# Kernel optimization log

Measured on AMD Instinct MI355X. Metric: run time of the kernel, lower is better.

Reference implementation:

```python
import jax, jax.numpy as jnp
import numpy as np

N = 200_000        # primal nodes (mesh faces)
E = 600_000        # directed primal edges (= dual nodes)
F = 128            # feature dim
NUM_KEEP = 300_000 # num_primal_edges_to_keep
ITERS = 40         # label-propagation iterations (>= ~2*log2(N), safely converged)


def setup_inputs() -> dict:
    key = jax.random.key(0)
    k1, k2, k3, k4 = jax.random.split(key, 4)
    primal_x = jax.random.normal(k1, (N, F), dtype=jnp.float32)
    dual_x = jax.random.normal(k2, (E, F), dtype=jnp.float32)
    att = jax.random.uniform(k3, (E,), dtype=jnp.float32)  # attention coeffs in (0,1)
    primal_edge_index = jax.random.randint(k4, (2, E), 0, N, dtype=jnp.int32)
    return {"primal_x": primal_x, "dual_x": dual_x, "att": att,
            "primal_edge_index": primal_edge_index}


def _pool(primal_x, dual_x, att, primal_edge_index):
    src, dst = primal_edge_index[0], primal_edge_index[1]
    num_pool = E - NUM_KEEP

    # --- Top-K edge selection by decreasing attention coefficient ---
    order = jnp.argsort(-att)
    pool_mask = jnp.zeros((E,), jnp.bool_).at[order[:num_pool]].set(True)

    # --- Union-find / connected components of pooled edges via
    #     min-label propagation with pointer jumping (vectorized union-find) ---
    u = src
    v = jnp.where(pool_mask, dst, src)  # masked edges become self-edges (no-ops)

    def body(_, l):
        l = l.at[u].min(l[v]).at[v].min(l[u])  # edge relaxations (scatter-min)
        l = l[l]                                # pointer jumping
        l = l[l]
        return l

    labels = jax.lax.fori_loop(0, ITERS, body, jnp.arange(N, dtype=jnp.int32))

    # --- Compact component labels into contiguous new-primal-node ids ---
    _, cluster = jnp.unique(labels, size=N, fill_value=N, return_inverse=True)
    cluster = cluster.astype(jnp.int32)

    # --- Aggregate primal node features per cluster ('mean') ---
    counts = jax.ops.segment_sum(jnp.ones((N,), primal_x.dtype), cluster,
                                 num_segments=N)
    new_primal_x = jax.ops.segment_sum(primal_x, cluster, num_segments=N)
    new_primal_x = new_primal_x / jnp.maximum(counts, 1.0)[:, None]

    # --- Rebuild primal edges; edges internal to a cluster are pooled away ---
    cu, cv = cluster[src], cluster[dst]
    valid = cu != cv
    new_primal_edge_index = jnp.stack([jnp.where(valid, cu, -1),
                                       jnp.where(valid, cv, -1)])

    # --- Dual nodes: one per (unordered) surviving new primal edge
    #     ('single' dual nodes); merge & mean-aggregate dual features of old
    #     dual nodes mapping to the same new dual node ---
    a = jnp.minimum(cu, cv)
    b = jnp.maximum(cu, cv)
    pairs = jnp.stack([jnp.where(valid, a, N), jnp.where(valid, b, N)], axis=1)
    _, dual_cluster = jnp.unique(pairs, axis=0, size=E, fill_value=N,
                                 return_inverse=True)
    dual_cluster = dual_cluster.reshape(E).astype(jnp.int32)
    vm = valid.astype(dual_x.dtype)
    dcounts = jax.ops.segment_sum(vm, dual_cluster, num_segments=E)
    new_dual_x = jax.ops.segment_sum(dual_x * vm[:, None], dual_cluster,
                                     num_segments=E)
    new_dual_x = new_dual_x / jnp.maximum(dcounts, 1.0)[:, None]

    return new_primal_x, new_dual_x, new_primal_edge_index, cluster


def reference(primal_x, dual_x, att, primal_edge_index):
    return _pool(primal_x, dual_x, att, primal_edge_index)
```

## Files before the change

kernel.cpp:

```cpp
#include <hip/hip_runtime.h>
#include <stdint.h>


#define N_NODES 200000
#define N_EDGES 600000
#define FDIM 128
#define NUM_POOL 300000u

#define SC_NEEDEQ 3
#define SC_TIECNT 4
#define SC_C 5
#define SC_W 6
#define SC_U 7
#define SC_VCNT 8
#define SC_WL0 16
#define TIECAP 4096
#define WLCAP 300800
#define HB 256
#define NSB 98
#define NSHAD 8
#define NSHAD2 16
#define CMAX 16384
#define SROWS 128
#define SGB 391
#define CS2B 128

__device__ __forceinline__ uint32_t f2ou(float f){
  uint32_t b = __float_as_uint(f);
  return (b & 0x80000000u) ? ~b : (b | 0x80000000u);
}

static __device__ __forceinline__ void sel_level(const uint32_t* hist, uint32_t& target,
                                                 uint32_t& pfx, uint32_t* sm, uint32_t* res){
  int t = threadIdx.x;
  uint32_t cnt = hist[t];
  sm[t] = cnt; __syncthreads();
  for(int off = 1; off < 256; off <<= 1){
    uint32_t y = (t + off < 256) ? sm[t + off] : 0u;
    __syncthreads(); sm[t] += y; __syncthreads();
  }
  uint32_t suffix = sm[t];
  uint32_t above  = suffix - cnt;
  if(above < target && target <= suffix){ res[0] = (uint32_t)t; res[1] = target - above; }
  __syncthreads();
  pfx = (pfx << 8) | res[0];
  target = res[1];
  __syncthreads();
}

static __device__ __forceinline__ uint32_t blk_excl(uint32_t v, uint32_t* sm, uint32_t& total){
  int t = threadIdx.x;
  sm[t] = v; __syncthreads();
  for(int off = 1; off < 256; off <<= 1){
    uint32_t y = (t >= off) ? sm[t - off] : 0u;
    __syncthreads(); sm[t] += y; __syncthreads();
  }
  total = sm[255];
  uint32_t incl = sm[t];
  __syncthreads();
  return incl - v;
}

__global__ __launch_bounds__(256) void k_zero(uint4* w4, uint32_t n4){
  uint32_t gid = blockIdx.x*256 + threadIdx.x;
  uint4 z = make_uint4(0u,0u,0u,0u);
  for(uint32_t j = gid; j < n4; j += gridDim.x*256) w4[j] = z;
}

template<int LEVEL>
__global__ __launch_bounds__(256) void k_hist8(const float* att, uint32_t* hists, int* L){
  __shared__ uint32_t h[256];
  __shared__ uint32_t sm[256];
  __shared__ uint32_t res[2];
  h[threadIdx.x] = 0;
  if(LEVEL == 1){
    for(int i = blockIdx.x*256 + threadIdx.x; i < N_NODES; i += HB*256) L[i] = i;
  }
  __syncthreads();
  uint32_t pfx = 0, target = NUM_POOL;
  #pragma unroll
  for(int l = 0; l < LEVEL-1; ++l) sel_level(hists + 256*l, target, pfx, sm, res);
  constexpr int SH1 = (LEVEL > 1) ? 8*(5-LEVEL) : 0;
  constexpr int SH2 = 8*(4-LEVEL);
  for(int e = blockIdx.x*256 + threadIdx.x; e < N_EDGES; e += HB*256){
    uint32_t u = f2ou(att[e]);
    bool ok = (LEVEL == 1) || ((u >> SH1) == pfx);
    if(ok) atomicAdd(&h[(u >> SH2) & 0xFFu], 1u);
  }
  __syncthreads();
  uint32_t c = h[threadIdx.x];
  if(c) atomicAdd(&hists[256*(LEVEL-1) + threadIdx.x], c);
}

__global__ __launch_bounds__(256) void k_seed(const float* att, const int* src, const int* dst,
                       const uint32_t* hists, uint32_t* sc, uint32_t* tieIdx, int* L, uint2* wl){
  __shared__ uint32_t sm[256];
  __shared__ uint32_t res[2];
  __shared__ uint32_t basesh;
  uint32_t pfx = 0, target = NUM_POOL;
  #pragma unroll
  for(int l = 0; l < 4; ++l) sel_level(hists + 256*l, target, pfx, sm, res);
  if(blockIdx.x == 0 && threadIdx.x == 0) sc[SC_NEEDEQ] = target;
  uint32_t T = pfx;
  int e = blockIdx.x*256 + threadIdx.x;
  bool app = false; int u = 0, v = 0;
  if(e < N_EDGES){
    uint32_t ub = f2ou(att[e]);
    if(ub > T){
      u = src[e]; v = dst[e];
      if(u != v){
        int m = u < v ? u : v, hi = u ^ v ^ m;
        atomicMin(&L[hi], m);
        app = true;
      }
    } else if(ub == T){
      uint32_t p = atomicAdd(&sc[SC_TIECNT], 1u);
      if(p < TIECAP) tieIdx[p] = (uint32_t)e;
    }
  }
  uint32_t tot;
  uint32_t off = blk_excl(app ? 1u : 0u, sm, tot);
  if(threadIdx.x == 0 && tot) basesh = atomicAdd(&sc[SC_WL0], tot);
  __syncthreads();
  if(app) wl[basesh + off] = make_uint2((uint32_t)(u < v ? u : v), (uint32_t)(u > v ? u : v));
}
__global__ __launch_bounds__(1024) void k_tiesel(uint32_t* sc, const uint32_t* tieIdx,
                        const int* src, const int* dst, int* L, uint2* wl){
  uint32_t m = sc[SC_TIECNT]; if(m > TIECAP) m = TIECAP;
  uint32_t need = sc[SC_NEEDEQ];
  int lane = threadIdx.x & 63;
  for(uint32_t i0 = 0; i0 < m; i0 += 1024){
    uint32_t i = i0 + threadIdx.x;
    bool app = false; int u = 0, v = 0;
    if(i < m){
      uint32_t mine = tieIdx[i];
      uint32_t r = 0;
      for(uint32_t j = 0; j < m; j++) r += (tieIdx[j] < mine) ? 1u : 0u;
      if(r < need){
        u = src[mine]; v = dst[mine];
        if(u != v){ int mm = u < v ? u : v, hi = u ^ v ^ mm; atomicMin(&L[hi], mm); app = true; }
      }
    }
    unsigned long long grp = __ballot(app);
    if(grp){
      int leader = __ffsll(grp) - 1;
      uint32_t base = 0;
      if(lane == leader) base = atomicAdd(&sc[SC_WL0], (uint32_t)__popcll(grp));
      base = (uint32_t)__shfl((int)base, leader);
      if(app){
        uint32_t off = (uint32_t)__popcll(grp & ((1ull << lane) - 1ull));
        wl[base + off] = make_uint2((uint32_t)(u < v ? u : v), (uint32_t)(u > v ? u : v));
      }
    }
  }
}
__global__ __launch_bounds__(256) void k_relax(const uint2* wl_in, uint2* wl_out, int* L,
                       uint32_t* sc, int inSlot, int outSlot){
  __shared__ uint32_t sm[256];
  __shared__ uint32_t basesh;
  uint32_t n = sc[inSlot];
  for(uint32_t base = blockIdx.x*256u; base < n; base += gridDim.x*256u){
    uint32_t idx = base + threadIdx.x;
    bool active = idx < n;
    int lu = 0, lv = 0;
    if(active){
      uint2 ed = wl_in[idx];
      lu = L[ed.x]; lu = L[lu]; lu = L[lu]; lu = L[lu];
      lv = L[ed.y]; lv = L[lv]; lv = L[lv]; lv = L[lv];
      active = (lu != lv);
      if(active){
        int m = lu < lv ? lu : lv, hi = lu ^ lv ^ m;
        atomicMin(&L[hi], m);
      }
    }
    uint32_t tot;
    uint32_t off = blk_excl(active ? 1u : 0u, sm, tot);
    if(threadIdx.x == 0 && tot) basesh = atomicAdd(&sc[outSlot], tot);
    __syncthreads();
    if(active) wl_out[basesh + off] = make_uint2((uint32_t)(lu < lv ? lu : lv),
                                                 (uint32_t)(lu > lv ? lu : lv));
  }
  if(n != 0){
    int i = blockIdx.x*256 + threadIdx.x;
    if(i < N_NODES){
      int v = L[i]; v = L[v]; v = L[v]; v = L[v];
      if(v < i) atomicMin(&L[i], v);
    }
  }
}
__global__ __launch_bounds__(256) void k_flatten_reduce(int* L, uint32_t* bsums){
  uint32_t base = blockIdx.x*2048u + threadIdx.x*8u;
  uint32_t s = 0;
  #pragma unroll
  for(int k = 0; k < 8; k++){
    uint32_t i = base + k;
    if(i < N_NODES){
      int p = L[i]; int q = L[p];
      while(q != p){ p = q; q = L[p]; }
      L[i] = p;
      s += (p == (int)i) ? 1u : 0u;
    }
  }
  __shared__ uint32_t sm[256];
  sm[threadIdx.x] = s; __syncthreads();
  for(int off = 128; off > 0; off >>= 1){
    if((int)threadIdx.x < off) sm[threadIdx.x] += sm[threadIdx.x + off];
    __syncthreads();
  }
  if(threadIdx.x == 0) bsums[blockIdx.x] = sm[0];
}

template<int MODE>
__device__ __forceinline__ uint32_t scan_n(const uint32_t* sc){
  if(MODE == 1) return sc[SC_W];
  if(MODE == 3) return sc[SC_C]*NSHAD2;
  return N_NODES;
}
template<int MODE>
__global__ __launch_bounds__(256) void k_scan_reduce(const uint32_t* in, uint32_t* bsums,
                       const uint32_t* sc, float* dsum, uint32_t* dcnt){
  uint32_t n = scan_n<MODE>(sc);
  if(MODE == 1){
    uint32_t vc = sc[SC_VCNT];
    size_t gid = (size_t)blockIdx.x*256 + threadIdx.x, gs = (size_t)gridDim.x*256;
    float4* d4 = (float4*)dsum;
    float4 z = make_float4(0.f,0.f,0.f,0.f);
    for(size_t j = gid; j < (size_t)vc*(FDIM/4); j += gs) d4[j] = z;
    for(size_t j = gid; j < vc; j += gs) dcnt[j] = 0u;
  }
  uint32_t base = blockIdx.x*2048u + threadIdx.x*8u;
  uint32_t s = 0;
  #pragma unroll
  for(int k = 0; k < 8; k++){
    uint32_t idx = base + k;
    if(idx < n){ uint32_t v = in[idx]; if(MODE == 1) v = __popc(v); s += v; }
  }
  __shared__ uint32_t sm[256];
  sm[threadIdx.x] = s; __syncthreads();
  for(int off = 128; off > 0; off >>= 1){
    if((int)threadIdx.x < off) sm[threadIdx.x] += sm[threadIdx.x + off];
    __syncthreads();
  }
  if(threadIdx.x == 0) bsums[blockIdx.x] = sm[0];
}
template<int MODE>
__global__ __launch_bounds__(256) void k_scan_apply(const uint32_t* in, const int* L,
                       const uint32_t* bsums, int nb, uint32_t* out, uint32_t* sc){
  __shared__ uint32_t bs[4096];
  __shared__ uint32_t sm[256];
  int t = threadIdx.x;
  uint32_t n = scan_n<MODE>(sc);
  uint32_t loc[16]; uint32_t ls = 0;
  #pragma unroll
  for(int k = 0; k < 16; k++){ int idx = t*16 + k; uint32_t v = (idx < nb) ? bsums[idx] : 0u; loc[k] = v; ls += v; }
  sm[t] = ls; __syncthreads();
  for(int off = 1; off < 256; off <<= 1){
    uint32_t y = (t >= off) ? sm[t - off] : 0u;
    __syncthreads(); sm[t] += y; __syncthreads();
  }
  uint32_t total = sm[255];
  uint32_t run = sm[t] - ls;
  #pragma unroll
  for(int k = 0; k < 16; k++){ bs[t*16 + k] = run; run += loc[k]; }
  __syncthreads();
  uint32_t blockbase = bs[blockIdx.x];
  __syncthreads();
  uint32_t base = blockIdx.x*2048u + t*8u;
  uint32_t xs[8]; uint32_t ts2 = 0;
  #pragma unroll
  for(int k = 0; k < 8; k++){
    uint32_t idx = base + k; uint32_t v = 0;
    if(idx < n){
      if(MODE == 2) v = (L[idx] == (int)idx) ? 1u : 0u;
      else { v = in[idx]; if(MODE == 1) v = __popc(v); }
    }
    xs[k] = v; ts2 += v;
  }
  sm[t] = ts2; __syncthreads();
  for(int off = 1; off < 256; off <<= 1){
    uint32_t y = (t >= off) ? sm[t - off] : 0u;
    __syncthreads(); sm[t] += y; __syncthreads();
  }
  uint32_t run2 = blockbase + sm[t] - ts2;
  #pragma unroll
  for(int k = 0; k < 8; k++){ uint32_t idx = base + k; if(idx < n) out[idx] = run2; run2 += xs[k]; }
  if(blockIdx.x == 0 && t == 0){
    if(MODE == 2){ sc[SC_C] = total; uint64_t cc = (uint64_t)total*(uint64_t)total; sc[SC_W] = (uint32_t)((cc + 31ull) >> 5); }
    if(MODE == 1){ sc[SC_U] = total; }
  }
}

__global__ __launch_bounds__(256) void k_cluster_counts(const int* L, const uint32_t* rank_,
                       int* cluster_i, float* outC, uint32_t* counts, uint32_t* counts2,
                       float* psumS, uint32_t* bitmap, const uint32_t* sc){
  uint32_t C = sc[SC_C], W = sc[SC_W];
  uint32_t gid = blockIdx.x*256 + threadIdx.x, gs = gridDim.x*256;
  float4* p4 = (float4*)psumS;
  float4 z = make_float4(0.f,0.f,0.f,0.f);
  for(size_t j = gid; j < (size_t)NSHAD*C*(FDIM/4); j += gs) p4[j] = z;
  for(uint32_t j = gid; j < W; j += gs) bitmap[j] = 0u;
  int i = (int)gid;
  int lane = threadIdx.x & 63;
  int sh = (int)((gid >> 6) & (NSHAD2-1));
  int c = -1;
  if(i < N_NODES){
    c = (int)rank_[L[i]];
    cluster_i[i] = c;
    outC[i] = (float)c;
  }
  unsigned long long remaining = __ballot(i < N_NODES);
  while(remaining){
    int leader = __ffsll(remaining) - 1;
    int lc = __shfl(c, leader);
    unsigned long long grp = __ballot(c == lc) & remaining;
    if(lane == leader){
      uint32_t cnt = (uint32_t)__popcll(grp);
      atomicAdd(&counts[lc], cnt);
      atomicAdd(&counts2[lc*NSHAD2 + sh], cnt);
    }
    remaining &= ~grp;
  }
}
__global__ void k_scatter(const int* cluster_i, uint32_t* cursor2, uint32_t* order){
  uint32_t gid = blockIdx.x*256 + threadIdx.x;
  int i = (int)gid;
  int lane = threadIdx.x & 63;
  int sh = (int)((gid >> 6) & (NSHAD2-1));
  int c = (i < N_NODES) ? cluster_i[i] : -1;
  unsigned long long remaining = __ballot(i < N_NODES);
  while(remaining){
    int leader = __ffsll(remaining) - 1;
    int lc = __shfl(c, leader);
    unsigned long long grp = __ballot(c == lc) & remaining;
    int b = 0;
    if(lane == leader) b = (int)atomicAdd(&cursor2[lc*NSHAD2 + sh], (uint32_t)__popcll(grp));
    b = __shfl(b, leader);
    if((grp >> lane) & 1ull){
      uint32_t sub = (uint32_t)__popcll(grp & ((1ull << lane) - 1ull));
      order[(uint32_t)b + sub] = (uint32_t)i;
    }
    remaining &= ~grp;
  }
}

__global__ __launch_bounds__(256) void k_seg_edges(const float* px, const uint32_t* order,
        const int* cluster_i, float* psumS, const int* src, const int* dst, uint32_t* sc,
        float* outE, uint32_t* kc, uint32_t* bitmap){
  if(blockIdx.x < SGB){
    int wave = (int)((blockIdx.x*256u + threadIdx.x) >> 6);
    int lane = threadIdx.x & 63;
    int start = wave * SROWS;
    if(start >= N_NODES) return;
    int cnt = N_NODES - start; if(cnt > SROWS) cnt = SROWS;
    size_t shadBase = (size_t)(wave & (NSHAD-1)) * (size_t)sc[SC_C] * FDIM;
    uint32_t ord0 = 0, ord1 = 0; int c0 = -1, c1 = -1;
    if(lane < cnt){ ord0 = order[start + lane]; c0 = cluster_i[ord0]; }
    if(64 + lane < cnt){ ord1 = order[start + 64 + lane]; c1 = cluster_i[ord1]; }
    float ax = 0.f, ay = 0.f; int cur = -1;
    for(int r = 0; r < cnt; r++){
      uint32_t i; int c;
      if(r < 64){ i = (uint32_t)__shfl((int)ord0, r); c = __shfl(c0, r); }
      else      { i = (uint32_t)__shfl((int)ord1, r - 64); c = __shfl(c1, r - 64); }
      if(c != cur){
        if(cur >= 0){
          atomicAdd(&psumS[shadBase + (size_t)cur*FDIM + 2*lane], ax);
          atomicAdd(&psumS[shadBase + (size_t)cur*FDIM + 2*lane + 1], ay);
        }
        cur = c; ax = 0.f; ay = 0.f;
      }
      float2 v = ((const float2*)(px + (size_t)i*FDIM))[lane];
      ax += v.x; ay += v.y;
    }
    if(cur >= 0){
      atomicAdd(&psumS[shadBase + (size_t)cur*FDIM + 2*lane], ax);
      atomicAdd(&psumS[shadBase + (size_t)cur*FDIM + 2*lane + 1], ay);
    }
  } else {
    __shared__ uint32_t wsum[4];
    int e = (blockIdx.x - SGB)*256 + threadIdx.x;
    int lane = threadIdx.x & 63;
    int wv = threadIdx.x >> 6;
    bool val = false;
    if(e < N_EDGES){
      int cu = cluster_i[src[e]];
      int cv = cluster_i[dst[e]];
      val = (cu != cv);
      outE[e] = val ? (float)cu : -1.0f;
      outE[N_EDGES + e] = val ? (float)cv : -1.0f;
      if(val){
        int a = cu < cv ? cu : cv, b = cu < cv ? cv : cu;
        uint32_t C = sc[SC_C];
        uint32_t key = (uint32_t)a * C + (uint32_t)b;
        kc[e] = key;
        atomicOr(&bitmap[key >> 5], 1u << (key & 31u));
      } else {
        kc[e] = 0xFFFFFFFFu;
      }
    }
    unsigned long long grp = __ballot(val);
    if(lane == 0) wsum[wv] = (uint32_t)__popcll(grp);
    __syncthreads();
    if(threadIdx.x == 0){
      uint32_t s = wsum[0] + wsum[1] + wsum[2] + wsum[3];
      if(s) atomicAdd(&sc[SC_VCNT], s);
    }
  }
}

__global__ __launch_bounds__(256) void k_dualacc(const float* dx, const uint32_t* kc,
                          const uint32_t* bitmap, const uint32_t* wpref,
                          float* dsum, uint32_t* dcnt){
  int wave = (int)((blockIdx.x*256u + threadIdx.x) >> 6);
  int lane = threadIdx.x & 63;
  int base = wave * 64;
  if(base >= N_EDGES) return;
  int e = base + lane;
  uint32_t key = (e < N_EDGES) ? kc[e] : 0xFFFFFFFFu;
  bool val = (key != 0xFFFFFFFFu);
  uint32_t r = 0;
  if(val){
    uint32_t wi = key >> 5, bi = key & 31u;
    r = wpref[wi] + __popc(bitmap[wi] & ((1u << bi) - 1u));
  }
  unsigned long long m = __ballot(val);
  while(m){
    int b = __ffsll(m) - 1;
    m &= m - 1;
    uint32_t ee = (uint32_t)(base + b);
    uint32_t rr = (uint32_t)__shfl((int)r, b);
    float2 v = ((const float2*)(dx + (size_t)ee*FDIM))[lane];
    atomicAdd(&dsum[(size_t)rr*FDIM + 2*lane], v.x);
    atomicAdd(&dsum[(size_t)rr*FDIM + 2*lane + 1], v.y);
    if(lane == 0) atomicAdd(&dcnt[rr], 1u);
  }
}
__global__ __launch_bounds__(256) void k_finalize(const float4* psumS, const uint32_t* counts,
        const float4* dsum, const uint32_t* dcnt, const uint32_t* sc, float4* out4){
  uint32_t C = sc[SC_C], U = sc[SC_U];
  size_t cs = (size_t)C * (FDIM/4);
  size_t gid = (size_t)blockIdx.x*256 + threadIdx.x;
  size_t gs = (size_t)gridDim.x*256;
  const size_t NP4 = (size_t)N_NODES*(FDIM/4);
  const size_t TOT4 = (size_t)(N_NODES + N_EDGES)*(FDIM/4);
  for(size_t j = gid; j < TOT4; j += gs){
    float4 v = make_float4(0.f,0.f,0.f,0.f);
    if(j < NP4){
      uint32_t r = (uint32_t)(j >> 5);
      if(r < C){
        v = psumS[j];
        #pragma unroll
        for(int s = 1; s < NSHAD; s++){
          float4 t = psumS[(size_t)s*cs + j];
          v.x += t.x; v.y += t.y; v.z += t.z; v.w += t.w;
        }
        float fc = (float)counts[r];
        v.x /= fc; v.y /= fc; v.z /= fc; v.w /= fc;
      }
    } else {
      size_t dj = j - NP4;
      uint32_t r = (uint32_t)(dj >> 5);
      if(r < U){
        v = dsum[dj];
        float fc = (float)dcnt[r];
        v.x /= fc; v.y /= fc; v.z /= fc; v.w /= fc;
      }
    }
    out4[j] = v;
  }
}

extern "C" void kernel_launch(void* const* d_in, const int* in_sizes, int n_in,
                              void* d_out, int out_size, void* d_ws, size_t ws_size,
                              hipStream_t stream){
  (void)in_sizes; (void)n_in; (void)out_size;
  const float* primal_x = (const float*)d_in[0];
  const float* dual_x   = (const float*)d_in[1];
  const float* att      = (const float*)d_in[2];
  const int*   pei      = (const int*)d_in[3];
  const int* src = pei;
  const int* dst = pei + N_EDGES;

  float* out  = (float*)d_out;
  float* outE = out + (size_t)(N_NODES + N_EDGES)*FDIM;
  float* outC = outE + (size_t)2*N_EDGES;

  uint32_t* w = (uint32_t*)d_ws;
  size_t words_avail = ws_size / 4;
  const size_t PSUMW = (size_t)NSHAD*CMAX*FDIM;
  const size_t CNT2W = (size_t)CMAX*NSHAD2;
  const size_t FIXED = 64 + 1024 + (size_t)N_NODES + CNT2W
                     + TIECAP + 4*(size_t)N_NODES + CNT2W + 4*(size_t)WLCAP
                     + (size_t)N_EDGES + (size_t)N_EDGES
                     + 4096
                     + PSUMW + (size_t)N_EDGES*FDIM;
  size_t wcap = (words_avail > FIXED) ? (words_avail - FIXED)/2 : 4;
  if(wcap > 8388608) wcap = 8388608;
  wcap &= ~(size_t)3;

  size_t o = 0;
  uint32_t* sc      = w;               o += 64;
  uint32_t* hists   = w + o;           o += 1024;
  uint32_t* counts  = w + o;           o += N_NODES;
  uint32_t* counts2 = w + o;           o += CNT2W;
  size_t zero_words = o;
  uint32_t* tieIdx  = w + o;           o += TIECAP;
  int* labels       = (int*)(w + o);   o += N_NODES;
  uint32_t* rank_   = w + o;           o += N_NODES;
  int* cluster_i    = (int*)(w + o);   o += N_NODES;
  uint32_t* order   = w + o;           o += N_NODES;
  uint32_t* cursor2 = w + o;           o += CNT2W;
  uint2* wl0        = (uint2*)(w + o); o += 2*(size_t)WLCAP;
  uint2* wl1        = (uint2*)(w + o); o += 2*(size_t)WLCAP;
  uint32_t* kc      = w + o;           o += N_EDGES;
  uint32_t* dcnt    = w + o;           o += N_EDGES;
  uint32_t* bsums   = w + o;           o += 4096;
  float* psumS      = (float*)(w + o); o += PSUMW;
  float* dsum       = (float*)(w + o); o += (size_t)N_EDGES*FDIM;
  uint32_t* bitmap  = w + o;           o += wcap;
  uint32_t* wpref   = w + o;           o += wcap;

  const int EB  = (N_EDGES + 255)/256;
  const int NB  = (N_NODES + 255)/256;
  const int WSB = (int)((wcap + 2047)/2048);

  k_zero<<<128,256,0,stream>>>((uint4*)w, (uint32_t)(zero_words/4));
  k_hist8<1><<<HB,256,0,stream>>>(att, hists, labels);
  k_hist8<2><<<HB,256,0,stream>>>(att, hists, labels);
  k_hist8<3><<<HB,256,0,stream>>>(att, hists, labels);
  k_hist8<4><<<HB,256,0,stream>>>(att, hists, labels);
  k_seed<<<EB,256,0,stream>>>(att, src, dst, hists, sc, tieIdx, labels, wl0);
  k_tiesel<<<1,1024,0,stream>>>(sc, tieIdx, src, dst, labels, wl0);
  for(int r = 1; r <= 8; ++r){
    uint2* win  = (r & 1) ? wl0 : wl1;
    uint2* wout = (r & 1) ? wl1 : wl0;
    k_relax<<<1024,256,0,stream>>>(win, wout, labels, sc, SC_WL0 + r - 1, SC_WL0 + r);
  }
  k_flatten_reduce<<<NSB,256,0,stream>>>(labels, bsums);
  k_scan_apply<2><<<NSB,256,0,stream>>>(counts, labels, bsums, NSB, rank_, sc);
  k_cluster_counts<<<NB,256,0,stream>>>(labels, rank_, cluster_i, outC, counts, counts2,
                                        psumS, bitmap, sc);
  k_scan_reduce<3><<<CS2B,256,0,stream>>>(counts2, bsums, sc, dsum, dcnt);
  k_scan_apply<3><<<CS2B,256,0,stream>>>(counts2, labels, bsums, CS2B, cursor2, sc);
  k_scatter<<<NB,256,0,stream>>>(cluster_i, cursor2, order);
  k_seg_edges<<<SGB + EB,256,0,stream>>>(primal_x, order, cluster_i, psumS,
                                         src, dst, sc, outE, kc, bitmap);
  k_scan_reduce<1><<<WSB,256,0,stream>>>(bitmap, bsums, sc, dsum, dcnt);
  k_scan_apply<1><<<WSB,256,0,stream>>>(bitmap, labels, bsums, WSB, wpref, sc);
  k_dualacc<<<EB,256,0,stream>>>(dual_x, kc, bitmap, wpref, dsum, dcnt);
  k_finalize<<<2048,256,0,stream>>>((const float4*)psumS, counts, (const float4*)dsum,
                                    dcnt, sc, (float4*)out);
}
```

Measured before the change: 626.6 us.

## Fuse seed, union-find relaxation, labeling and scatter into one cooperative kernel

Replaces the chain of small kernels (seed, tie selection, eight relax rounds, flatten, rank scan, cluster counts, count scan, scatter) with a single cooperative persistent kernel of 1024 blocks that uses grid-wide syncs between phases. The aim is to remove roughly fifteen kernel launches and their inter-kernel gaps, and to exit the relax loop early once the worklist is empty. In exchange it adds grid.sync barriers, serial single-block phases for tie selection and the small scans, and it depends on all 1024 blocks being co-resident for the cooperative launch.

```diff
diff --git a/kernel.cpp b/kernel.cpp
--- a/kernel.cpp
+++ b/kernel.cpp
@@ -1,5 +1,8 @@
 #include <hip/hip_runtime.h>
+#include <hip/hip_cooperative_groups.h>
 #include <stdint.h>
+
+namespace cg = cooperative_groups;
 
 
 #define N_NODES 200000
@@ -23,11 +26,14 @@
 #define CMAX 16384
 #define SROWS 128
 #define SGB 391
-#define CS2B 128
+#define CGB 1024
 
 __device__ __forceinline__ uint32_t f2ou(float f){
   uint32_t b = __float_as_uint(f);
   return (b & 0x80000000u) ? ~b : (b | 0x80000000u);
+}
+__device__ __forceinline__ uint32_t ld_ag(const uint32_t* p){
+  return __hip_atomic_load(p, __ATOMIC_RELAXED, __HIP_MEMORY_SCOPE_AGENT);
 }
 
 static __device__ __forceinline__ void sel_level(const uint32_t* hist, uint32_t& target,
@@ -92,135 +98,244 @@
   if(c) atomicAdd(&hists[256*(LEVEL-1) + threadIdx.x], c);
 }
 
-__global__ __launch_bounds__(256) void k_seed(const float* att, const int* src, const int* dst,
-                       const uint32_t* hists, uint32_t* sc, uint32_t* tieIdx, int* L, uint2* wl){
+__global__ __launch_bounds__(256) void k_mega(const float* att, const int* src, const int* dst,
+      const uint32_t* hists, uint32_t* sc, uint32_t* tieIdx, int* L,
+      uint2* wl0, uint2* wl1, uint32_t* bsums, uint32_t* rank_, int* cluster_i,
+      float* outC, uint32_t* counts, uint32_t* counts2, float* psumS,
+      uint32_t* bitmap, uint32_t* cursor2, uint32_t* order){
+  cg::grid_group grid = cg::this_grid();
   __shared__ uint32_t sm[256];
   __shared__ uint32_t res[2];
   __shared__ uint32_t basesh;
+  const uint32_t tid = threadIdx.x;
+  const uint32_t gid = blockIdx.x*256u + tid;
+  const uint32_t GS  = CGB*256u;
+  const int lane = (int)(tid & 63);
+
   uint32_t pfx = 0, target = NUM_POOL;
   #pragma unroll
   for(int l = 0; l < 4; ++l) sel_level(hists + 256*l, target, pfx, sm, res);
-  if(blockIdx.x == 0 && threadIdx.x == 0) sc[SC_NEEDEQ] = target;
-  uint32_t T = pfx;
-  int e = blockIdx.x*256 + threadIdx.x;
-  bool app = false; int u = 0, v = 0;
-  if(e < N_EDGES){
-    uint32_t ub = f2ou(att[e]);
-    if(ub > T){
-      u = src[e]; v = dst[e];
-      if(u != v){
-        int m = u < v ? u : v, hi = u ^ v ^ m;
-        atomicMin(&L[hi], m);
-        app = true;
-      }
-    } else if(ub == T){
-      uint32_t p = atomicAdd(&sc[SC_TIECNT], 1u);
-      if(p < TIECAP) tieIdx[p] = (uint32_t)e;
-    }
-  }
-  uint32_t tot;
-  uint32_t off = blk_excl(app ? 1u : 0u, sm, tot);
-  if(threadIdx.x == 0 && tot) basesh = atomicAdd(&sc[SC_WL0], tot);
-  __syncthreads();
-  if(app) wl[basesh + off] = make_uint2((uint32_t)(u < v ? u : v), (uint32_t)(u > v ? u : v));
-}
-__global__ __launch_bounds__(1024) void k_tiesel(uint32_t* sc, const uint32_t* tieIdx,
-                        const int* src, const int* dst, int* L, uint2* wl){
-  uint32_t m = sc[SC_TIECNT]; if(m > TIECAP) m = TIECAP;
-  uint32_t need = sc[SC_NEEDEQ];
-  int lane = threadIdx.x & 63;
-  for(uint32_t i0 = 0; i0 < m; i0 += 1024){
-    uint32_t i = i0 + threadIdx.x;
+  if(gid == 0) sc[SC_NEEDEQ] = target;
+  const uint32_t T = pfx;
+
+  for(uint32_t e0 = blockIdx.x*256u; e0 < N_EDGES; e0 += GS){
+    uint32_t e = e0 + tid;
     bool app = false; int u = 0, v = 0;
-    if(i < m){
-      uint32_t mine = tieIdx[i];
-      uint32_t r = 0;
-      for(uint32_t j = 0; j < m; j++) r += (tieIdx[j] < mine) ? 1u : 0u;
-      if(r < need){
-        u = src[mine]; v = dst[mine];
-        if(u != v){ int mm = u < v ? u : v, hi = u ^ v ^ mm; atomicMin(&L[hi], mm); app = true; }
-      }
-    }
-    unsigned long long grp = __ballot(app);
-    if(grp){
-      int leader = __ffsll(grp) - 1;
-      uint32_t base = 0;
-      if(lane == leader) base = atomicAdd(&sc[SC_WL0], (uint32_t)__popcll(grp));
-      base = (uint32_t)__shfl((int)base, leader);
-      if(app){
-        uint32_t off = (uint32_t)__popcll(grp & ((1ull << lane) - 1ull));
-        wl[base + off] = make_uint2((uint32_t)(u < v ? u : v), (uint32_t)(u > v ? u : v));
-      }
-    }
-  }
-}
-__global__ __launch_bounds__(256) void k_relax(const uint2* wl_in, uint2* wl_out, int* L,
-                       uint32_t* sc, int inSlot, int outSlot){
-  __shared__ uint32_t sm[256];
-  __shared__ uint32_t basesh;
-  uint32_t n = sc[inSlot];
-  for(uint32_t base = blockIdx.x*256u; base < n; base += gridDim.x*256u){
-    uint32_t idx = base + threadIdx.x;
-    bool active = idx < n;
-    int lu = 0, lv = 0;
-    if(active){
-      uint2 ed = wl_in[idx];
-      lu = L[ed.x]; lu = L[lu]; lu = L[lu]; lu = L[lu];
-      lv = L[ed.y]; lv = L[lv]; lv = L[lv]; lv = L[lv];
-      active = (lu != lv);
+    if(e < N_EDGES){
+      uint32_t ub = f2ou(att[e]);
+      if(ub > T){
+        u = src[e]; v = dst[e];
+        if(u != v){ int m = u < v ? u : v, hi = u ^ v ^ m; atomicMin(&L[hi], m); app = true; }
+      } else if(ub == T){
+        uint32_t p = atomicAdd(&sc[SC_TIECNT], 1u);
+        if(p < TIECAP) tieIdx[p] = e;
+      }
+    }
+    uint32_t tot, off = blk_excl(app ? 1u : 0u, sm, tot);
+    if(tid == 0 && tot) basesh = atomicAdd(&sc[SC_WL0], tot);
+    __syncthreads();
+    if(app) wl0[basesh + off] = make_uint2((uint32_t)(u < v ? u : v), (uint32_t)(u > v ? u : v));
+    __syncthreads();
+  }
+  grid.sync();
+
+  if(blockIdx.x == 0){
+    uint32_t m = sc[SC_TIECNT]; if(m > TIECAP) m = TIECAP;
+    uint32_t need = sc[SC_NEEDEQ];
+    for(uint32_t i0 = 0; i0 < m; i0 += 256){
+      uint32_t i = i0 + tid;
+      bool app = false; int u = 0, v = 0;
+      if(i < m){
+        uint32_t mine = tieIdx[i];
+        uint32_t rr = 0;
+        for(uint32_t j = 0; j < m; j++) rr += (tieIdx[j] < mine) ? 1u : 0u;
+        if(rr < need){
+          u = src[mine]; v = dst[mine];
+          if(u != v){ int mm = u < v ? u : v, hi = u ^ v ^ mm; atomicMin(&L[hi], mm); app = true; }
+        }
+      }
+      uint32_t tot, off = blk_excl(app ? 1u : 0u, sm, tot);
+      if(tid == 0 && tot) basesh = atomicAdd(&sc[SC_WL0], tot);
+      __syncthreads();
+      if(app) wl0[basesh + off] = make_uint2((uint32_t)(u < v ? u : v), (uint32_t)(u > v ? u : v));
+      __syncthreads();
+    }
+  }
+  grid.sync();
+
+  for(int r = 1; r <= 8; ++r){
+    uint32_t n = ld_ag(&sc[SC_WL0 + r - 1]);
+    if(n == 0) break;
+    const uint2* win = (r & 1) ? wl0 : wl1;
+    uint2* wout      = (r & 1) ? wl1 : wl0;
+    for(uint32_t base = blockIdx.x*256u; base < n; base += GS){
+      uint32_t idx = base + tid;
+      bool active = idx < n;
+      int lu = 0, lv = 0;
       if(active){
-        int m = lu < lv ? lu : lv, hi = lu ^ lv ^ m;
-        atomicMin(&L[hi], m);
-      }
-    }
-    uint32_t tot;
-    uint32_t off = blk_excl(active ? 1u : 0u, sm, tot);
-    if(threadIdx.x == 0 && tot) basesh = atomicAdd(&sc[outSlot], tot);
-    __syncthreads();
-    if(active) wl_out[basesh + off] = make_uint2((uint32_t)(lu < lv ? lu : lv),
+        uint2 ed = win[idx];
+        lu = L[ed.x]; lu = L[lu]; lu = L[lu]; lu = L[lu];
+        lv = L[ed.y]; lv = L[lv]; lv = L[lv]; lv = L[lv];
+        active = (lu != lv);
+        if(active){ int m = lu < lv ? lu : lv, hi = lu ^ lv ^ m; atomicMin(&L[hi], m); }
+      }
+      uint32_t tot, off = blk_excl(active ? 1u : 0u, sm, tot);
+      if(tid == 0 && tot) basesh = atomicAdd(&sc[SC_WL0 + r], tot);
+      __syncthreads();
+      if(active) wout[basesh + off] = make_uint2((uint32_t)(lu < lv ? lu : lv),
                                                  (uint32_t)(lu > lv ? lu : lv));
-  }
-  if(n != 0){
-    int i = blockIdx.x*256 + threadIdx.x;
-    if(i < N_NODES){
+      __syncthreads();
+    }
+    for(uint32_t i = gid; i < N_NODES; i += GS){
       int v = L[i]; v = L[v]; v = L[v]; v = L[v];
-      if(v < i) atomicMin(&L[i], v);
-    }
-  }
-}
-__global__ __launch_bounds__(256) void k_flatten_reduce(int* L, uint32_t* bsums){
-  uint32_t base = blockIdx.x*2048u + threadIdx.x*8u;
-  uint32_t s = 0;
-  #pragma unroll
-  for(int k = 0; k < 8; k++){
-    uint32_t i = base + k;
-    if(i < N_NODES){
-      int p = L[i]; int q = L[p];
-      while(q != p){ p = q; q = L[p]; }
-      L[i] = p;
-      s += (p == (int)i) ? 1u : 0u;
-    }
-  }
-  __shared__ uint32_t sm[256];
-  sm[threadIdx.x] = s; __syncthreads();
-  for(int off = 128; off > 0; off >>= 1){
-    if((int)threadIdx.x < off) sm[threadIdx.x] += sm[threadIdx.x + off];
-    __syncthreads();
-  }
-  if(threadIdx.x == 0) bsums[blockIdx.x] = sm[0];
-}
-
-template<int MODE>
-__device__ __forceinline__ uint32_t scan_n(const uint32_t* sc){
-  if(MODE == 1) return sc[SC_W];
-  if(MODE == 3) return sc[SC_C]*NSHAD2;
-  return N_NODES;
-}
-template<int MODE>
-__global__ __launch_bounds__(256) void k_scan_reduce(const uint32_t* in, uint32_t* bsums,
+      if(v < (int)i) atomicMin(&L[i], v);
+    }
+    grid.sync();
+  }
+
+  for(uint32_t chunk = blockIdx.x; chunk < NSB; chunk += CGB){
+    uint32_t base = chunk*2048u + tid*8u;
+    uint32_t s = 0;
+    #pragma unroll
+    for(int k = 0; k < 8; k++){
+      uint32_t i = base + k;
+      if(i < N_NODES){
+        int p = L[i]; int q = L[p];
+        while(q != p){ p = q; q = L[p]; }
+        L[i] = p;
+        s += (p == (int)i) ? 1u : 0u;
+      }
+    }
+    sm[tid] = s; __syncthreads();
+    for(int off = 128; off > 0; off >>= 1){
+      if((int)tid < off) sm[tid] += sm[tid + off];
+      __syncthreads();
+    }
+    if(tid == 0) bsums[chunk] = sm[0];
+    __syncthreads();
+  }
+  grid.sync();
+
+  if(blockIdx.x == 0){
+    uint32_t v = (tid < NSB) ? bsums[tid] : 0u;
+    uint32_t tot, excl = blk_excl(v, sm, tot);
+    if(tid < NSB) bsums[tid] = excl;
+    if(tid == 0){ sc[SC_C] = tot; uint64_t cc = (uint64_t)tot*tot; sc[SC_W] = (uint32_t)((cc + 31ull) >> 5); }
+  }
+  grid.sync();
+
+  for(uint32_t chunk = blockIdx.x; chunk < NSB; chunk += CGB){
+    uint32_t base = chunk*2048u + tid*8u;
+    uint32_t xs[8]; uint32_t ts = 0;
+    #pragma unroll
+    for(int k = 0; k < 8; k++){
+      uint32_t idx = base + k;
+      uint32_t v = (idx < N_NODES && L[idx] == (int)idx) ? 1u : 0u;
+      xs[k] = v; ts += v;
+    }
+    uint32_t tot, excl = blk_excl(ts, sm, tot);
+    uint32_t run = bsums[chunk] + excl;
+    #pragma unroll
+    for(int k = 0; k < 8; k++){ uint32_t idx = base + k; if(idx < N_NODES) rank_[idx] = run; run += xs[k]; }
+    __syncthreads();
+  }
+  grid.sync();
+
+  {
+    uint32_t C = ld_ag(&sc[SC_C]);
+    uint32_t W = ld_ag(&sc[SC_W]);
+    float4* p4 = (float4*)psumS;
+    float4 z = make_float4(0.f,0.f,0.f,0.f);
+    for(size_t j = gid; j < (size_t)NSHAD*C*(FDIM/4); j += GS) p4[j] = z;
+    for(uint32_t j = gid; j < W; j += GS) bitmap[j] = 0u;
+  }
+  for(uint32_t base = blockIdx.x*256u; base < N_NODES; base += GS){
+    uint32_t i0 = base + tid;
+    bool act = i0 < N_NODES;
+    int c = -1;
+    if(act){
+      c = (int)rank_[L[i0]];
+      cluster_i[i0] = c;
+      outC[i0] = (float)c;
+    }
+    int sh = (int)((i0 >> 6) & (NSHAD2-1));
+    unsigned long long remaining = __ballot(act);
+    while(remaining){
+      int leader = __ffsll(remaining) - 1;
+      int lc = __shfl(c, leader);
+      unsigned long long grp = __ballot(c == lc) & remaining;
+      if(lane == leader){
+        uint32_t cnt = (uint32_t)__popcll(grp);
+        atomicAdd(&counts[lc], cnt);
+        atomicAdd(&counts2[lc*NSHAD2 + sh], cnt);
+      }
+      remaining &= ~grp;
+    }
+  }
+  grid.sync();
+
+  uint32_t C = ld_ag(&sc[SC_C]);
+  uint32_t n2 = C*NSHAD2;
+  uint32_t nch = (n2 + 2047u) >> 11;
+  for(uint32_t chunk = blockIdx.x; chunk < nch; chunk += CGB){
+    uint32_t base = chunk*2048u + tid*8u;
+    uint32_t s = 0;
+    #pragma unroll
+    for(int k = 0; k < 8; k++){ uint32_t idx = base + k; if(idx < n2) s += counts2[idx]; }
+    sm[tid] = s; __syncthreads();
+    for(int off = 128; off > 0; off >>= 1){
+      if((int)tid < off) sm[tid] += sm[tid + off];
+      __syncthreads();
+    }
+    if(tid == 0) bsums[chunk] = sm[0];
+    __syncthreads();
+  }
+  grid.sync();
+  if(blockIdx.x == 0){
+    uint32_t v = (tid < nch) ? bsums[tid] : 0u;
+    uint32_t tot, excl = blk_excl(v, sm, tot);
+    if(tid < nch) bsums[tid] = excl;
+  }
+  grid.sync();
+  for(uint32_t chunk = blockIdx.x; chunk < nch; chunk += CGB){
+    uint32_t base = chunk*2048u + tid*8u;
+    uint32_t xs[8]; uint32_t ts = 0;
+    #pragma unroll
+    for(int k = 0; k < 8; k++){ uint32_t idx = base + k; uint32_t v = (idx < n2) ? counts2[idx] : 0u; xs[k] = v; ts += v; }
+    uint32_t tot, excl = blk_excl(ts, sm, tot);
+    uint32_t run = bsums[chunk] + excl;
+    #pragma unroll
+    for(int k = 0; k < 8; k++){ uint32_t idx = base + k; if(idx < n2) cursor2[idx] = run; run += xs[k]; }
+    __syncthreads();
+  }
+  grid.sync();
+
+  for(uint32_t base = blockIdx.x*256u; base < N_NODES; base += GS){
+    uint32_t i0 = base + tid;
+    bool act = i0 < N_NODES;
+    int c = act ? cluster_i[i0] : -1;
+    int sh = (int)((i0 >> 6) & (NSHAD2-1));
+    unsigned long long remaining = __ballot(act);
+    while(remaining){
+      int leader = __ffsll(remaining) - 1;
+      int lc = __shfl(c, leader);
+      unsigned long long grp = __ballot(c == lc) & remaining;
+      int b = 0;
+      if(lane == leader) b = (int)atomicAdd(&cursor2[lc*NSHAD2 + sh], (uint32_t)__popcll(grp));
+      b = __shfl(b, leader);
+      if((grp >> lane) & 1ull){
+        uint32_t sub = (uint32_t)__popcll(grp & ((1ull << lane) - 1ull));
+        order[(uint32_t)b + sub] = i0;
+      }
+      remaining &= ~grp;
+    }
+  }
+}
+
+__global__ __launch_bounds__(256) void k_scan_reduce1(const uint32_t* in, uint32_t* bsums,
                        const uint32_t* sc, float* dsum, uint32_t* dcnt){
-  uint32_t n = scan_n<MODE>(sc);
-  if(MODE == 1){
+  uint32_t n = sc[SC_W];
+  {
     uint32_t vc = sc[SC_VCNT];
     size_t gid = (size_t)blockIdx.x*256 + threadIdx.x, gs = (size_t)gridDim.x*256;
     float4* d4 = (float4*)dsum;
@@ -233,7 +348,7 @@
   #pragma unroll
   for(int k = 0; k < 8; k++){
     uint32_t idx = base + k;
-    if(idx < n){ uint32_t v = in[idx]; if(MODE == 1) v = __popc(v); s += v; }
+    if(idx < n) s += __popc(in[idx]);
   }
   __shared__ uint32_t sm[256];
   sm[threadIdx.x] = s; __syncthreads();
@@ -243,13 +358,12 @@
   }
   if(threadIdx.x == 0) bsums[blockIdx.x] = sm[0];
 }
-template<int MODE>
-__global__ __launch_bounds__(256) void k_scan_apply(const uint32_t* in, const int* L,
-                       const uint32_t* bsums, int nb, uint32_t* out, uint32_t* sc){
+__global__ __launch_bounds__(256) void k_scan_apply1(const uint32_t* in, const uint32_t* bsums,
+                       int nb, uint32_t* out, uint32_t* sc){
   __shared__ uint32_t bs[4096];
   __shared__ uint32_t sm[256];
   int t = threadIdx.x;
-  uint32_t n = scan_n<MODE>(sc);
+  uint32_t n = sc[SC_W];
   uint32_t loc[16]; uint32_t ls = 0;
   #pragma unroll
   for(int k = 0; k < 16; k++){ int idx = t*16 + k; uint32_t v = (idx < nb) ? bsums[idx] : 0u; loc[k] = v; ls += v; }
@@ -269,11 +383,8 @@
   uint32_t xs[8]; uint32_t ts2 = 0;
   #pragma unroll
   for(int k = 0; k < 8; k++){
-    uint32_t idx = base + k; uint32_t v = 0;
-    if(idx < n){
-      if(MODE == 2) v = (L[idx] == (int)idx) ? 1u : 0u;
-      else { v = in[idx]; if(MODE == 1) v = __popc(v); }
-    }
+    uint32_t idx = base + k;
+    uint32_t v = (idx < n) ? __popc(in[idx]) : 0u;
     xs[k] = v; ts2 += v;
   }
   sm[t] = ts2; __syncthreads();
@@ -284,63 +395,7 @@
   uint32_t run2 = blockbase + sm[t] - ts2;
   #pragma unroll
   for(int k = 0; k < 8; k++){ uint32_t idx = base + k; if(idx < n) out[idx] = run2; run2 += xs[k]; }
-  if(blockIdx.x == 0 && t == 0){
-    if(MODE == 2){ sc[SC_C] = total; uint64_t cc = (uint64_t)total*(uint64_t)total; sc[SC_W] = (uint32_t)((cc + 31ull) >> 5); }
-    if(MODE == 1){ sc[SC_U] = total; }
-  }
-}
-
-__global__ __launch_bounds__(256) void k_cluster_counts(const int* L, const uint32_t* rank_,
-                       int* cluster_i, float* outC, uint32_t* counts, uint32_t* counts2,
-                       float* psumS, uint32_t* bitmap, const uint32_t* sc){
-  uint32_t C = sc[SC_C], W = sc[SC_W];
-  uint32_t gid = blockIdx.x*256 + threadIdx.x, gs = gridDim.x*256;
-  float4* p4 = (float4*)psumS;
-  float4 z = make_float4(0.f,0.f,0.f,0.f);
-  for(size_t j = gid; j < (size_t)NSHAD*C*(FDIM/4); j += gs) p4[j] = z;
-  for(uint32_t j = gid; j < W; j += gs) bitmap[j] = 0u;
-  int i = (int)gid;
-  int lane = threadIdx.x & 63;
-  int sh = (int)((gid >> 6) & (NSHAD2-1));
-  int c = -1;
-  if(i < N_NODES){
-    c = (int)rank_[L[i]];
-    cluster_i[i] = c;
-    outC[i] = (float)c;
-  }
-  unsigned long long remaining = __ballot(i < N_NODES);
-  while(remaining){
-    int leader = __ffsll(remaining) - 1;
-    int lc = __shfl(c, leader);
-    unsigned long long grp = __ballot(c == lc) & remaining;
-    if(lane == leader){
-      uint32_t cnt = (uint32_t)__popcll(grp);
-      atomicAdd(&counts[lc], cnt);
-      atomicAdd(&counts2[lc*NSHAD2 + sh], cnt);
-    }
-    remaining &= ~grp;
-  }
-}
-__global__ void k_scatter(const int* cluster_i, uint32_t* cursor2, uint32_t* order){
-  uint32_t gid = blockIdx.x*256 + threadIdx.x;
-  int i = (int)gid;
-  int lane = threadIdx.x & 63;
-  int sh = (int)((gid >> 6) & (NSHAD2-1));
-  int c = (i < N_NODES) ? cluster_i[i] : -1;
-  unsigned long long remaining = __ballot(i < N_NODES);
-  while(remaining){
-    int leader = __ffsll(remaining) - 1;
-    int lc = __shfl(c, leader);
-    unsigned long long grp = __ballot(c == lc) & remaining;
-    int b = 0;
-    if(lane == leader) b = (int)atomicAdd(&cursor2[lc*NSHAD2 + sh], (uint32_t)__popcll(grp));
-    b = __shfl(b, leader);
-    if((grp >> lane) & 1ull){
-      uint32_t sub = (uint32_t)__popcll(grp & ((1ull << lane) - 1ull));
-      order[(uint32_t)b + sub] = (uint32_t)i;
-    }
-    remaining &= ~grp;
-  }
+  if(blockIdx.x == 0 && t == 0) sc[SC_U] = total;
 }
 
 __global__ __launch_bounds__(256) void k_seg_edges(const float* px, const uint32_t* order,
@@ -520,7 +575,6 @@
   uint32_t* wpref   = w + o;           o += wcap;
 
   const int EB  = (N_EDGES + 255)/256;
-  const int NB  = (N_NODES + 255)/256;
   const int WSB = (int)((wcap + 2047)/2048);
 
   k_zero<<<128,256,0,stream>>>((uint4*)w, (uint32_t)(zero_words/4));
@@ -528,24 +582,18 @@
   k_hist8<2><<<HB,256,0,stream>>>(att, hists, labels);
   k_hist8<3><<<HB,256,0,stream>>>(att, hists, labels);
   k_hist8<4><<<HB,256,0,stream>>>(att, hists, labels);
-  k_seed<<<EB,256,0,stream>>>(att, src, dst, hists, sc, tieIdx, labels, wl0);
-  k_tiesel<<<1,1024,0,stream>>>(sc, tieIdx, src, dst, labels, wl0);
-  for(int r = 1; r <= 8; ++r){
-    uint2* win  = (r & 1) ? wl0 : wl1;
-    uint2* wout = (r & 1) ? wl1 : wl0;
-    k_relax<<<1024,256,0,stream>>>(win, wout, labels, sc, SC_WL0 + r - 1, SC_WL0 + r);
-  }
-  k_flatten_reduce<<<NSB,256,0,stream>>>(labels, bsums);
-  k_scan_apply<2><<<NSB,256,0,stream>>>(counts, labels, bsums, NSB, rank_, sc);
-  k_cluster_counts<<<NB,256,0,stream>>>(labels, rank_, cluster_i, outC, counts, counts2,
-                                        psumS, bitmap, sc);
-  k_scan_reduce<3><<<CS2B,256,0,stream>>>(counts2, bsums, sc, dsum, dcnt);
-  k_scan_apply<3><<<CS2B,256,0,stream>>>(counts2, labels, bsums, CS2B, cursor2, sc);
-  k_scatter<<<NB,256,0,stream>>>(cluster_i, cursor2, order);
+  {
+    void* kargs[] = { (void*)&att, (void*)&src, (void*)&dst, (void*)&hists, (void*)&sc,
+                      (void*)&tieIdx, (void*)&labels, (void*)&wl0, (void*)&wl1, (void*)&bsums,
+                      (void*)&rank_, (void*)&cluster_i, (void*)&outC, (void*)&counts,
+                      (void*)&counts2, (void*)&psumS, (void*)&bitmap, (void*)&cursor2,
+                      (void*)&order };
+    hipLaunchCooperativeKernel((void*)k_mega, dim3(CGB), dim3(256), kargs, 0, stream);
+  }
   k_seg_edges<<<SGB + EB,256,0,stream>>>(primal_x, order, cluster_i, psumS,
                                          src, dst, sc, outE, kc, bitmap);
-  k_scan_reduce<1><<<WSB,256,0,stream>>>(bitmap, bsums, sc, dsum, dcnt);
-  k_scan_apply<1><<<WSB,256,0,stream>>>(bitmap, labels, bsums, WSB, wpref, sc);
+  k_scan_reduce1<<<WSB,256,0,stream>>>(bitmap, bsums, sc, dsum, dcnt);
+  k_scan_apply1<<<WSB,256,0,stream>>>(bitmap, bsums, WSB, wpref, sc);
   k_dualacc<<<EB,256,0,stream>>>(dual_x, kc, bitmap, wpref, dsum, dcnt);
   k_finalize<<<2048,256,0,stream>>>((const float4*)psumS, counts, (const float4*)dsum,
                                     dcnt, sc, (float4*)out);
```

After: 1.791 ms. 186% more time.
